# Kernel optimization log

Measured on AMD Instinct MI355X. Metric: run time of the kernel, lower is better.

Reference implementation:

```python
import jax, jax.numpy as jnp
import numpy as np


def _pairwise_iou(boxes):
    x1, y1, x2, y2 = boxes[:, 0], boxes[:, 1], boxes[:, 2], boxes[:, 3]
    area = (x2 - x1 + 1.0) * (y2 - y1 + 1.0)                       # [N]
    xx1 = jnp.maximum(x1[:, None], x1[None, :])                    # [N,N]
    yy1 = jnp.maximum(y1[:, None], y1[None, :])
    xx2 = jnp.minimum(x2[:, None], x2[None, :])
    yy2 = jnp.minimum(y2[:, None], y2[None, :])
    w = jnp.maximum(xx2 - xx1 + 1.0, 0.0)
    h = jnp.maximum(yy2 - yy1 + 1.0, 0.0)
    inter = w * h
    return inter / (area[:, None] + area[None, :] - inter)


def setup_inputs() -> dict:
    key = jax.random.key(0)
    k1, k2, k3 = jax.random.split(key, 3)
    N = 8192
    CANVAS, MAX_WH = 1000.0, 200.0
    xy = jax.random.uniform(k1, (N, 2), dtype=jnp.float32) * CANVAS
    wh = jax.random.uniform(k2, (N, 2), dtype=jnp.float32) * MAX_WH + 1.0
    scores = jax.random.uniform(k3, (N, 1), dtype=jnp.float32)
    dets = jnp.concatenate([xy, xy + wh, scores], axis=1)  # [N,5] = x1,y1,x2,y2,score
    return {"dets": dets, "threshold": 0.7}


def reference(dets, threshold):
    # Greedy NMS: sort by score desc, sequentially suppress later boxes with IoU > thr.
    scores = dets[:, 4]
    order = jnp.argsort(-scores)                 # [N] descending-score permutation
    boxes = dets[order, :4]                      # [N,4] sorted boxes
    iou = _pairwise_iou(boxes)                   # [N,N]
    N = boxes.shape[0]
    idx = jnp.arange(N)

    def body(i, suppressed):
        alive = jnp.logical_not(suppressed[i])
        newly = alive & (iou[i] > threshold) & (idx > i)
        return suppressed | newly

    suppressed = jax.lax.fori_loop(0, N, body, jnp.zeros((N,), dtype=bool))
    keep_sorted = jnp.logical_not(suppressed)    # keep mask in score order
    # Map keep mask back to original box order (fixed-shape stand-in for the
    # variable-length index list the torch kernel returns).
    keep = jnp.zeros((N,), dtype=bool).at[order].set(keep_sorted)
    # Return kept detections (suppressed rows zeroed) -> fixed output shape [N,5].
    return dets * keep[:, None].astype(dets.dtype)
```

## Files before the change

### kernel.cpp

```cpp
#include <hip/hip_runtime.h>
#include <stdint.h>
#include <math.h>

typedef unsigned long long u64;
typedef unsigned int u32;

#define ENT_CAP  8192
#define GCAP     65536
#define LDSE_CAP 24576

__global__ void k_scores(const float* __restrict__ dets, float* __restrict__ sc,
                         int* __restrict__ cnt, int n) {
    int i = blockIdx.x * blockDim.x + threadIdx.x;
    if (i < n) sc[i] = dets[i * 5 + 4];
    if (i < 129) cnt[i] = 0;
}

__global__ void k_rank(const float* __restrict__ dets, const float* __restrict__ sc,
                       int* __restrict__ rank,
                       float* __restrict__ sx1, float* __restrict__ sy1,
                       float* __restrict__ sx2, float* __restrict__ sy2,
                       float* __restrict__ sarea, int n) {
    int gid  = blockIdx.x * blockDim.x + threadIdx.x;
    int grp  = gid >> 6;
    int lane = threadIdx.x & 63;
    int i0 = grp * 4;
    if (i0 >= n) return;

    float s0 = sc[i0];
    float s1 = (i0 + 1 < n) ? sc[i0 + 1] : 0.0f;
    float s2 = (i0 + 2 < n) ? sc[i0 + 2] : 0.0f;
    float s3 = (i0 + 3 < n) ? sc[i0 + 3] : 0.0f;

    int c0 = 0, c1 = 0, c2 = 0, c3 = 0;
    int n4 = n >> 2;
    const float4* sc4 = (const float4*)sc;
    for (int j4 = lane; j4 < n4; j4 += 64) {
        float4 v = sc4[j4];
        int j = j4 * 4;
        c0 += (v.x > s0) || (v.x == s0 && (j + 0) < i0);
        c0 += (v.y > s0) || (v.y == s0 && (j + 1) < i0);
        c0 += (v.z > s0) || (v.z == s0 && (j + 2) < i0);
        c0 += (v.w > s0) || (v.w == s0 && (j + 3) < i0);
        c1 += (v.x > s1) || (v.x == s1 && (j + 0) < i0 + 1);
        c1 += (v.y > s1) || (v.y == s1 && (j + 1) < i0 + 1);
        c1 += (v.z > s1) || (v.z == s1 && (j + 2) < i0 + 1);
        c1 += (v.w > s1) || (v.w == s1 && (j + 3) < i0 + 1);
        c2 += (v.x > s2) || (v.x == s2 && (j + 0) < i0 + 2);
        c2 += (v.y > s2) || (v.y == s2 && (j + 1) < i0 + 2);
        c2 += (v.z > s2) || (v.z == s2 && (j + 2) < i0 + 2);
        c2 += (v.w > s2) || (v.w == s2 && (j + 3) < i0 + 2);
        c3 += (v.x > s3) || (v.x == s3 && (j + 0) < i0 + 3);
        c3 += (v.y > s3) || (v.y == s3 && (j + 1) < i0 + 3);
        c3 += (v.z > s3) || (v.z == s3 && (j + 2) < i0 + 3);
        c3 += (v.w > s3) || (v.w == s3 && (j + 3) < i0 + 3);
    }
    for (int j = (n4 << 2) + lane; j < n; j += 64) {
        float sj = sc[j];
        c0 += (sj > s0) || (sj == s0 && j < i0);
        c1 += (sj > s1) || (sj == s1 && j < i0 + 1);
        c2 += (sj > s2) || (sj == s2 && j < i0 + 2);
        c3 += (sj > s3) || (sj == s3 && j < i0 + 3);
    }
    #pragma unroll
    for (int off = 32; off > 0; off >>= 1) {
        c0 += __shfl_xor(c0, off, 64);
        c1 += __shfl_xor(c1, off, 64);
        c2 += __shfl_xor(c2, off, 64);
        c3 += __shfl_xor(c3, off, 64);
    }
    if (lane < 4) {
        int i = i0 + lane;
        if (i < n) {
            int r = (lane == 0) ? c0 : (lane == 1) ? c1 : (lane == 2) ? c2 : c3;
            rank[i] = r;
            float x1 = dets[i * 5 + 0], y1 = dets[i * 5 + 1];
            float x2 = dets[i * 5 + 2], y2 = dets[i * 5 + 3];
            sx1[r] = x1; sy1[r] = y1; sx2[r] = x2; sy2[r] = y2;
            sarea[r] = (x2 - x1 + 1.0f) * (y2 - y1 + 1.0f);
        }
    }
}

__global__ void k_mask(const float* __restrict__ sx1, const float* __restrict__ sy1,
                       const float* __restrict__ sx2, const float* __restrict__ sy2,
                       const float* __restrict__ sarea, const float* __restrict__ thrp,
                       u64* __restrict__ diag, u64* __restrict__ nzarr,
                       u32* __restrict__ entc, u32* __restrict__ ent2,
                       int* __restrict__ cnt, int n, int nw) {
    int t = blockIdx.x;
    double nn = (double)nw + 0.5;
    int by = (int)(nn - sqrt(nn * nn - 2.0 * (double)t));
    if (by < 0) by = 0; if (by > nw - 1) by = nw - 1;
    while (by + 1 <= nw - 1 && ((by + 1) * nw - ((by + 1) * by) / 2) <= t) ++by;
    while ((by * nw - (by * (by - 1)) / 2) > t) --by;
    int bx = by + (t - (by * nw - (by * (by - 1)) / 2));

    int k  = threadIdx.x;
    int i  = by * 64 + k;

    __shared__ float cx1[64], cy1[64], cx2[64], cy2[64], ca[64];
    int j0 = bx * 64;
    cx1[k] = sx1[j0 + k]; cy1[k] = sy1[j0 + k];
    cx2[k] = sx2[j0 + k]; cy2[k] = sy2[j0 + k];
    ca[k]  = sarea[j0 + k];
    __syncthreads();

    float x1 = sx1[i], y1 = sy1[i], x2 = sx2[i], y2 = sy2[i], ar = sarea[i];
    float thr = *thrp;
    u64 word = 0ULL;
    #pragma unroll 8
    for (int jj = 0; jj < 64; ++jj) {
        float xx1 = fmaxf(x1, cx1[jj]);
        float yy1 = fmaxf(y1, cy1[jj]);
        float xx2 = fminf(x2, cx2[jj]);
        float yy2 = fminf(y2, cy2[jj]);
        float w = fmaxf(xx2 - xx1 + 1.0f, 0.0f);
        float h = fmaxf(yy2 - yy1 + 1.0f, 0.0f);
        float inter = w * h;
        float denom = ar + ca[jj] - inter;
        word |= ((u64)(inter > thr * denom)) << jj;
    }

    if (bx == by) {
        word &= ~((2ULL << k) - 1ULL);
        diag[i] = word;
        u64 bal = __ballot(word != 0ULL);
        if (k == 0) nzarr[by] = bal;
        return;
    }
    if (__ballot(word != 0ULL) == 0ULL) return;
    int pc = __popcll(word);
    if (pc) {
        int base2 = atomicAdd(&cnt[by], pc);
        int baseg = atomicAdd(&cnt[128], pc);
        u64 ww = word;
        int x = 0;
        while (ww) {
            int jj = __builtin_ctzll(ww); ww &= ww - 1;
            int j = j0 + jj;
            if (base2 + x < ENT_CAP)
                ent2[(size_t)by * ENT_CAP + base2 + x] = ((u32)k << 16) | (u32)j;
            if (n <= 8192 && baseg + x < GCAP)
                entc[baseg + x] = ((u32)by << 19) | ((u32)k << 13) | (u32)j;
            ++x;
        }
    }
}

__device__ __forceinline__ u64 readlane_u64(u64 v, int lane) {
    unsigned lo = (unsigned)__builtin_amdgcn_readlane((int)(v & 0xffffffffu), lane);
    unsigned hi = (unsigned)__builtin_amdgcn_readlane((int)(v >> 32), lane);
    return ((u64)hi << 32) | lo;
}

__launch_bounds__(64, 1)
__global__ void k_scan(const u64* __restrict__ diag, const u64* __restrict__ nzarr,
                       const u32* __restrict__ entc, const u32* __restrict__ ent2,
                       const int* __restrict__ cnt, u64* __restrict__ remv,
                       int n, int nw) {
    extern __shared__ char smem[];
    u64* lds_remv = (u64*)smem;
    int* lds_cur  = (int*)(smem + 1024);
    u32* lds_ent  = (u32*)(smem + 1536);

    int lane = threadIdx.x;
    lds_remv[lane] = 0ULL;
    lds_remv[64 + lane] = 0ULL;

    int c0 = cnt[lane];
    int c1 = cnt[64 + lane];
    int S  = cnt[128];
    u64 nz0 = (lane < nw)      ? nzarr[lane]      : 0ULL;
    u64 nz1 = (64 + lane < nw) ? nzarr[64 + lane] : 0ULL;

    int s0 = c0;
    #pragma unroll
    for (int d = 1; d < 64; d <<= 1) { int tv = __shfl_up(s0, d, 64); if (lane >= d) s0 += tv; }
    int tot0 = __builtin_amdgcn_readlane(s0, 63);
    int s1 = c1;
    #pragma unroll
    for (int d = 1; d < 64; d <<= 1) { int tv = __shfl_up(s1, d, 64); if (lane >= d) s1 += tv; }
    int o0 = s0 - c0;
    int o1 = tot0 + s1 - c1;

    bool fast = (S <= LDSE_CAP) && (n <= 8192);

    if (fast) {
        lds_cur[lane] = o0;
        lds_cur[64 + lane] = o1;
        for (int g0 = 0; g0 < S; g0 += 1024) {
            int base = g0 + lane * 16;
            uint4 v0 = *(const uint4*)(entc + base);
            uint4 v1 = *(const uint4*)(entc + base + 4);
            uint4 v2 = *(const uint4*)(entc + base + 8);
            uint4 v3 = *(const uint4*)(entc + base + 12);
            u32 ee[16] = { v0.x, v0.y, v0.z, v0.w, v1.x, v1.y, v1.z, v1.w,
                           v2.x, v2.y, v2.z, v2.w, v3.x, v3.y, v3.z, v3.w };
            #pragma unroll
            for (int u = 0; u < 16; ++u) {
                if (base + u < S) {
                    u32 e = ee[u];
                    int b = e >> 19;
                    int pos = atomicAdd(&lds_cur[b], 1);
                    lds_ent[pos] = e;
                }
            }
        }
    }

    for (int b = 0; b < nw; ++b) {
        int sel = b & 63;
        int cb  = __builtin_amdgcn_readlane((b < 64) ? c0 : c1, sel);
        u64 nzb = readlane_u64((b < 64) ? nz0 : nz1, sel);
        if ((nzb | (u64)(u32)cb) == 0ULL) continue;

        u64 w = lds_remv[b];
        if (nzb & ~w) {
            u64 avail = ~w & nzb;
            while (avail) {
                int k = __builtin_ctzll(avail);
                w |= diag[(size_t)b * 64 + k];
                avail &= ~(w | (1ULL << k));
            }
            if (lane == 0) lds_remv[b] = w;
        }
        int ob = __builtin_amdgcn_readlane((b < 64) ? o0 : o1, sel);
        if (fast) {
            for (int idx = lane; idx < cb; idx += 64) {
                u32 e = lds_ent[ob + idx];
                int k = (e >> 13) & 63, j = e & 8191;
                if (!((w >> k) & 1ULL)) atomicOr(&lds_remv[j >> 6], 1ULL << (j & 63));
            }
        } else {
            int cbl = (cb < ENT_CAP) ? cb : ENT_CAP;
            for (int idx = lane; idx < cbl; idx += 64) {
                u32 e = ent2[(size_t)b * ENT_CAP + idx];
                int k = e >> 16, j = e & 0xffff;
                if (!((w >> k) & 1ULL)) atomicOr(&lds_remv[j >> 6], 1ULL << (j & 63));
            }
        }
    }

    if (lane < nw) remv[lane] = lds_remv[lane];
    if (64 + lane < nw) remv[64 + lane] = lds_remv[64 + lane];
}

__global__ void k_out(const float* __restrict__ dets, const int* __restrict__ rank,
                      const u64* __restrict__ remv, float* __restrict__ out, int n) {
    int idx = blockIdx.x * blockDim.x + threadIdx.x;
    if (idx >= n * 5) return;
    int i = idx / 5;
    int r = rank[i];
    u64 w = remv[r >> 6];
    float keep = ((w >> (r & 63)) & 1ULL) ? 0.0f : 1.0f;
    out[idx] = dets[idx] * keep;
}

extern "C" void kernel_launch(void* const* d_in, const int* in_sizes, int n_in,
                              void* d_out, int out_size, void* d_ws, size_t ws_size,
                              hipStream_t stream) {
    const float* dets = (const float*)d_in[0];
    const float* thrp = (const float*)d_in[1];
    int n  = in_sizes[0] / 5;
    int nw = (n + 63) / 64;

    char* ws = (char*)d_ws;
    size_t off = 0;
    auto carve = [&](size_t bytes) { char* p = ws + off; off = (off + bytes + 255) & ~(size_t)255; return p; };
    u64* diag  = (u64*)carve((size_t)n * sizeof(u64));
    u64* nzarr = (u64*)carve(128 * sizeof(u64));
    u32* entc  = (u32*)carve((size_t)GCAP * sizeof(u32));
    u32* ent2  = (u32*)carve((size_t)128 * ENT_CAP * sizeof(u32));
    int* cnt   = (int*)carve(129 * sizeof(int));
    float* sc    = (float*)carve((size_t)n * sizeof(float));
    int*   rank  = (int*)  carve((size_t)n * sizeof(int));
    float* sx1   = (float*)carve((size_t)n * sizeof(float));
    float* sy1   = (float*)carve((size_t)n * sizeof(float));
    float* sx2   = (float*)carve((size_t)n * sizeof(float));
    float* sy2   = (float*)carve((size_t)n * sizeof(float));
    float* sarea = (float*)carve((size_t)n * sizeof(float));
    u64* remv    = (u64*)  carve((size_t)nw * sizeof(u64));

    float* out = (float*)d_out;

    int tri = nw * (nw + 1) / 2;
    int scan_lds = 1024 + 512 + LDSE_CAP * 4;
    int ngrp = (n + 3) / 4;

    k_scores<<<(n + 255) / 256, 256, 0, stream>>>(dets, sc, cnt, n);
    k_rank<<<(ngrp * 64 + 255) / 256, 256, 0, stream>>>(dets, sc, rank, sx1, sy1, sx2, sy2, sarea, n);
    k_mask<<<tri, 64, 0, stream>>>(sx1, sy1, sx2, sy2, sarea, thrp, diag, nzarr, entc, ent2, cnt, n, nw);
    k_scan<<<1, 64, scan_lds, stream>>>(diag, nzarr, entc, ent2, cnt, remv, n, nw);
    k_out<<<(n * 5 + 255) / 256, 256, 0, stream>>>(dets, rank, remv, out, n);
}
```

Before: 95.19 us.

## Drop global compact entry list; stage per-row entries into LDS directly

```diff
diff --git a/kernel.cpp b/kernel.cpp
--- a/kernel.cpp
+++ b/kernel.cpp
@@ -6,14 +6,13 @@
 typedef unsigned int u32;
 
 #define ENT_CAP  8192
-#define GCAP     65536
 #define LDSE_CAP 24576
 
 __global__ void k_scores(const float* __restrict__ dets, float* __restrict__ sc,
                          int* __restrict__ cnt, int n) {
     int i = blockIdx.x * blockDim.x + threadIdx.x;
     if (i < n) sc[i] = dets[i * 5 + 4];
-    if (i < 129) cnt[i] = 0;
+    if (i < 128) cnt[i] = 0;
 }
 
 __global__ void k_rank(const float* __restrict__ dets, const float* __restrict__ sc,
@@ -24,15 +23,13 @@
     int gid  = blockIdx.x * blockDim.x + threadIdx.x;
     int grp  = gid >> 6;
     int lane = threadIdx.x & 63;
-    int i0 = grp * 4;
+    int i0 = grp * 2;
     if (i0 >= n) return;
 
     float s0 = sc[i0];
     float s1 = (i0 + 1 < n) ? sc[i0 + 1] : 0.0f;
-    float s2 = (i0 + 2 < n) ? sc[i0 + 2] : 0.0f;
-    float s3 = (i0 + 3 < n) ? sc[i0 + 3] : 0.0f;
-
-    int c0 = 0, c1 = 0, c2 = 0, c3 = 0;
+
+    int c0 = 0, c1 = 0;
     int n4 = n >> 2;
     const float4* sc4 = (const float4*)sc;
     for (int j4 = lane; j4 < n4; j4 += 64) {
@@ -46,33 +43,21 @@
         c1 += (v.y > s1) || (v.y == s1 && (j + 1) < i0 + 1);
         c1 += (v.z > s1) || (v.z == s1 && (j + 2) < i0 + 1);
         c1 += (v.w > s1) || (v.w == s1 && (j + 3) < i0 + 1);
-        c2 += (v.x > s2) || (v.x == s2 && (j + 0) < i0 + 2);
-        c2 += (v.y > s2) || (v.y == s2 && (j + 1) < i0 + 2);
-        c2 += (v.z > s2) || (v.z == s2 && (j + 2) < i0 + 2);
-        c2 += (v.w > s2) || (v.w == s2 && (j + 3) < i0 + 2);
-        c3 += (v.x > s3) || (v.x == s3 && (j + 0) < i0 + 3);
-        c3 += (v.y > s3) || (v.y == s3 && (j + 1) < i0 + 3);
-        c3 += (v.z > s3) || (v.z == s3 && (j + 2) < i0 + 3);
-        c3 += (v.w > s3) || (v.w == s3 && (j + 3) < i0 + 3);
     }
     for (int j = (n4 << 2) + lane; j < n; j += 64) {
         float sj = sc[j];
         c0 += (sj > s0) || (sj == s0 && j < i0);
         c1 += (sj > s1) || (sj == s1 && j < i0 + 1);
-        c2 += (sj > s2) || (sj == s2 && j < i0 + 2);
-        c3 += (sj > s3) || (sj == s3 && j < i0 + 3);
     }
     #pragma unroll
     for (int off = 32; off > 0; off >>= 1) {
         c0 += __shfl_xor(c0, off, 64);
         c1 += __shfl_xor(c1, off, 64);
-        c2 += __shfl_xor(c2, off, 64);
-        c3 += __shfl_xor(c3, off, 64);
-    }
-    if (lane < 4) {
+    }
+    if (lane < 2) {
         int i = i0 + lane;
         if (i < n) {
-            int r = (lane == 0) ? c0 : (lane == 1) ? c1 : (lane == 2) ? c2 : c3;
+            int r = lane ? c1 : c0;
             rank[i] = r;
             float x1 = dets[i * 5 + 0], y1 = dets[i * 5 + 1];
             float x2 = dets[i * 5 + 2], y2 = dets[i * 5 + 3];
@@ -86,8 +71,7 @@
                        const float* __restrict__ sx2, const float* __restrict__ sy2,
                        const float* __restrict__ sarea, const float* __restrict__ thrp,
                        u64* __restrict__ diag, u64* __restrict__ nzarr,
-                       u32* __restrict__ entc, u32* __restrict__ ent2,
-                       int* __restrict__ cnt, int n, int nw) {
+                       u32* __restrict__ ent2, int* __restrict__ cnt, int n, int nw) {
     int t = blockIdx.x;
     double nn = (double)nw + 0.5;
     int by = (int)(nn - sqrt(nn * nn - 2.0 * (double)t));
@@ -133,7 +117,6 @@
     int pc = __popcll(word);
     if (pc) {
         int base2 = atomicAdd(&cnt[by], pc);
-        int baseg = atomicAdd(&cnt[128], pc);
         u64 ww = word;
         int x = 0;
         while (ww) {
@@ -141,8 +124,6 @@
             int j = j0 + jj;
             if (base2 + x < ENT_CAP)
                 ent2[(size_t)by * ENT_CAP + base2 + x] = ((u32)k << 16) | (u32)j;
-            if (n <= 8192 && baseg + x < GCAP)
-                entc[baseg + x] = ((u32)by << 19) | ((u32)k << 13) | (u32)j;
             ++x;
         }
     }
@@ -156,13 +137,11 @@
 
 __launch_bounds__(64, 1)
 __global__ void k_scan(const u64* __restrict__ diag, const u64* __restrict__ nzarr,
-                       const u32* __restrict__ entc, const u32* __restrict__ ent2,
-                       const int* __restrict__ cnt, u64* __restrict__ remv,
-                       int n, int nw) {
+                       const u32* __restrict__ ent2, const int* __restrict__ cnt,
+                       u64* __restrict__ remv, int n, int nw) {
     extern __shared__ char smem[];
     u64* lds_remv = (u64*)smem;
-    int* lds_cur  = (int*)(smem + 1024);
-    u32* lds_ent  = (u32*)(smem + 1536);
+    u32* lds_ent  = (u32*)(smem + 1024);
 
     int lane = threadIdx.x;
     lds_remv[lane] = 0ULL;
@@ -170,7 +149,8 @@
 
     int c0 = cnt[lane];
     int c1 = cnt[64 + lane];
-    int S  = cnt[128];
+    c0 = (c0 < ENT_CAP) ? c0 : ENT_CAP;
+    c1 = (c1 < ENT_CAP) ? c1 : ENT_CAP;
     u64 nz0 = (lane < nw)      ? nzarr[lane]      : 0ULL;
     u64 nz1 = (64 + lane < nw) ? nzarr[64 + lane] : 0ULL;
 
@@ -181,38 +161,37 @@
     int s1 = c1;
     #pragma unroll
     for (int d = 1; d < 64; d <<= 1) { int tv = __shfl_up(s1, d, 64); if (lane >= d) s1 += tv; }
+    int tot1 = __builtin_amdgcn_readlane(s1, 63);
     int o0 = s0 - c0;
     int o1 = tot0 + s1 - c1;
-
-    bool fast = (S <= LDSE_CAP) && (n <= 8192);
+    int S  = tot0 + tot1;
+
+    bool fast = (S <= LDSE_CAP);
 
     if (fast) {
-        lds_cur[lane] = o0;
-        lds_cur[64 + lane] = o1;
-        for (int g0 = 0; g0 < S; g0 += 1024) {
-            int base = g0 + lane * 16;
-            uint4 v0 = *(const uint4*)(entc + base);
-            uint4 v1 = *(const uint4*)(entc + base + 4);
-            uint4 v2 = *(const uint4*)(entc + base + 8);
-            uint4 v3 = *(const uint4*)(entc + base + 12);
-            u32 ee[16] = { v0.x, v0.y, v0.z, v0.w, v1.x, v1.y, v1.z, v1.w,
-                           v2.x, v2.y, v2.z, v2.w, v3.x, v3.y, v3.z, v3.w };
+        for (int g = 0; g < nw; g += 8) {
+            u32 a[8]; int cbs[8], obs[8];
             #pragma unroll
-            for (int u = 0; u < 16; ++u) {
-                if (base + u < S) {
-                    u32 e = ee[u];
-                    int b = e >> 19;
-                    int pos = atomicAdd(&lds_cur[b], 1);
-                    lds_ent[pos] = e;
-                }
-            }
+            for (int u = 0; u < 8; ++u) {
+                int b = g + u;
+                bool lo = b < 64; int sel = b & 63;
+                cbs[u] = (b < nw) ? __builtin_amdgcn_readlane(lo ? c0 : c1, sel) : 0;
+                obs[u] = (b < nw) ? __builtin_amdgcn_readlane(lo ? o0 : o1, sel) : 0;
+                a[u] = (lane < cbs[u]) ? ent2[(size_t)b * ENT_CAP + lane] : 0u;
+            }
+            #pragma unroll
+            for (int u = 0; u < 8; ++u)
+                if (lane < cbs[u]) lds_ent[obs[u] + lane] = a[u];
+            for (int u = 0; u < 8; ++u)
+                for (int idx = 64 + lane; idx < cbs[u]; idx += 64)
+                    lds_ent[obs[u] + idx] = ent2[(size_t)(g + u) * ENT_CAP + idx];
         }
     }
 
     for (int b = 0; b < nw; ++b) {
-        int sel = b & 63;
-        int cb  = __builtin_amdgcn_readlane((b < 64) ? c0 : c1, sel);
-        u64 nzb = readlane_u64((b < 64) ? nz0 : nz1, sel);
+        int sel = b & 63; bool lo = b < 64;
+        int cb  = __builtin_amdgcn_readlane(lo ? c0 : c1, sel);
+        u64 nzb = readlane_u64(lo ? nz0 : nz1, sel);
         if ((nzb | (u64)(u32)cb) == 0ULL) continue;
 
         u64 w = lds_remv[b];
@@ -225,16 +204,15 @@
             }
             if (lane == 0) lds_remv[b] = w;
         }
-        int ob = __builtin_amdgcn_readlane((b < 64) ? o0 : o1, sel);
+        int ob = __builtin_amdgcn_readlane(lo ? o0 : o1, sel);
         if (fast) {
             for (int idx = lane; idx < cb; idx += 64) {
                 u32 e = lds_ent[ob + idx];
-                int k = (e >> 13) & 63, j = e & 8191;
+                int k = e >> 16, j = e & 0xffff;
                 if (!((w >> k) & 1ULL)) atomicOr(&lds_remv[j >> 6], 1ULL << (j & 63));
             }
         } else {
-            int cbl = (cb < ENT_CAP) ? cb : ENT_CAP;
-            for (int idx = lane; idx < cbl; idx += 64) {
+            for (int idx = lane; idx < cb; idx += 64) {
                 u32 e = ent2[(size_t)b * ENT_CAP + idx];
                 int k = e >> 16, j = e & 0xffff;
                 if (!((w >> k) & 1ULL)) atomicOr(&lds_remv[j >> 6], 1ULL << (j & 63));
@@ -270,9 +248,8 @@
     auto carve = [&](size_t bytes) { char* p = ws + off; off = (off + bytes + 255) & ~(size_t)255; return p; };
     u64* diag  = (u64*)carve((size_t)n * sizeof(u64));
     u64* nzarr = (u64*)carve(128 * sizeof(u64));
-    u32* entc  = (u32*)carve((size_t)GCAP * sizeof(u32));
     u32* ent2  = (u32*)carve((size_t)128 * ENT_CAP * sizeof(u32));
-    int* cnt   = (int*)carve(129 * sizeof(int));
+    int* cnt   = (int*)carve(128 * sizeof(int));
     float* sc    = (float*)carve((size_t)n * sizeof(float));
     int*   rank  = (int*)  carve((size_t)n * sizeof(int));
     float* sx1   = (float*)carve((size_t)n * sizeof(float));
@@ -285,12 +262,12 @@
     float* out = (float*)d_out;
 
     int tri = nw * (nw + 1) / 2;
-    int scan_lds = 1024 + 512 + LDSE_CAP * 4;
-    int ngrp = (n + 3) / 4;
+    int scan_lds = 1024 + LDSE_CAP * 4;
+    int ngrp = (n + 1) / 2;
 
     k_scores<<<(n + 255) / 256, 256, 0, stream>>>(dets, sc, cnt, n);
     k_rank<<<(ngrp * 64 + 255) / 256, 256, 0, stream>>>(dets, sc, rank, sx1, sy1, sx2, sy2, sarea, n);
-    k_mask<<<tri, 64, 0, stream>>>(sx1, sy1, sx2, sy2, sarea, thrp, diag, nzarr, entc, ent2, cnt, n, nw);
-    k_scan<<<1, 64, scan_lds, stream>>>(diag, nzarr, entc, ent2, cnt, remv, n, nw);
+    k_mask<<<tri, 64, 0, stream>>>(sx1, sy1, sx2, sy2, sarea, thrp, diag, nzarr, ent2, cnt, n, nw);
+    k_scan<<<1, 64, scan_lds, stream>>>(diag, nzarr, ent2, cnt, remv, n, nw);
     k_out<<<(n * 5 + 255) / 256, 256, 0, stream>>>(dets, rank, remv, out, n);
 }
```

After: 101.3 us. +6.4%, slower.
